# Performance work log

Hardware: AMD Instinct MI355X
Metric: run time of the kernel (lower is better)

The kernel has to match this reference:

```python
import jax, jax.numpy as jnp
import numpy as np


def setup_inputs() -> dict:
    key = jax.random.key(0)
    k1, k2 = jax.random.split(key)
    B, G = 32, 512
    center = jax.random.normal(k1, (B, G, 6), dtype=jnp.float32)
    lrf = jax.random.normal(k2, (B, G, 3, 3), dtype=jnp.float32)
    return {"center": center, "lrf": lrf}


def reference(center, lrf):
    # center: [B, G, 6], lrf: [B, G, 3, 3]
    center_pos = center[:, :, 0:3]                       # [B, G, 3]
    # diff[b, i, j, c] = center_pos[b, j, c] - center_pos[b, i, c]
    diff = center_pos[:, None, :, :] - center_pos[:, :, None, :]  # [B, G, G, 3]
    # rel_pos[b, i, j, k] = sum_c diff[b, i, j, c] * lrf[b, i, c, k]
    rel_pos = jnp.einsum('bijc,bick->bijk', diff, lrf)   # [B, G, G, 3]
    # rel_ori[b, i, j] = lrf[b, i]^T @ lrf[b, j]
    rel_ori = jnp.einsum('bikm,bjkn->bijmn', lrf, lrf)   # [B, G, G, 3, 3]
    return (rel_pos, rel_ori)
```

## Files before the change

kernel.cpp:

```cpp
#include <hip/hip_runtime.h>


#define G_ 512
#define NB 32

__global__ __launch_bounds__(256) void relposori_kernel(
    const float* __restrict__ center,
    const float* __restrict__ lrf,
    float* __restrict__ out_pos,
    float* __restrict__ out_ori)
{
    __shared__ float s[4 * 3072];
    int tid  = threadIdx.x;
    int lane = tid & 63;
    int w    = tid >> 6;
    float* sp = s + w * 3072;
    float* so = sp + 768;

    const int nchunks = NB * G_ * 2;
    const int nwaves  = gridDim.x * 4;
    int cw = blockIdx.x * 4 + w;

    for (int c = cw; c < nchunks; c += nwaves) {
        int bi = c >> 1;
        int b  = bi >> 9;
        int j0 = (c & 1) << 8;

        const float* ci = center + (size_t)bi * 6;
        const float* li = lrf    + (size_t)bi * 9;
        float ci0 = ci[0], ci1 = ci[1], ci2 = ci[2];
        float li_[9];
#pragma unroll
        for (int t = 0; t < 9; ++t) li_[t] = li[t];

#pragma unroll
        for (int q = 0; q < 4; ++q) {
            int jl = (q << 6) + lane;
            size_t bj = (size_t)b * G_ + (size_t)(j0 + jl);
            const float* cj = center + bj * 6;
            const float* lj = lrf    + bj * 9;
            float d0 = cj[0] - ci0, d1 = cj[1] - ci1, d2 = cj[2] - ci2;
            float lj_[9];
#pragma unroll
            for (int t = 0; t < 9; ++t) lj_[t] = lj[t];

#pragma unroll
            for (int k = 0; k < 3; ++k)
                sp[jl * 3 + k] = d0 * li_[k] + d1 * li_[3 + k] + d2 * li_[6 + k];

#pragma unroll
            for (int m = 0; m < 3; ++m)
#pragma unroll
                for (int n = 0; n < 3; ++n)
                    so[jl * 9 + m * 3 + n] = li_[m]     * lj_[n]
                                           + li_[3 + m] * lj_[3 + n]
                                           + li_[6 + m] * lj_[6 + n];
        }

        asm volatile("s_waitcnt lgkmcnt(0)" ::: "memory");
        __builtin_amdgcn_sched_barrier(0);

        size_t row = (size_t)bi * G_ + (size_t)j0;
        const float4* sp4 = (const float4*)sp;
        float4* op4 = (float4*)(out_pos + row * 3);
#pragma unroll
        for (int t = 0; t < 3; ++t)
            op4[(t << 6) + lane] = sp4[(t << 6) + lane];

        const float4* so4 = (const float4*)so;
        float4* oo4 = (float4*)(out_ori + row * 9);
#pragma unroll
        for (int t = 0; t < 9; ++t)
            oo4[(t << 6) + lane] = so4[(t << 6) + lane];

        asm volatile("" ::: "memory");
        __builtin_amdgcn_wave_barrier();
    }
}

extern "C" void kernel_launch(void* const* d_in, const int* in_sizes, int n_in,
                              void* d_out, int out_size, void* d_ws, size_t ws_size,
                              hipStream_t stream) {
    const float* center = (const float*)d_in[0];
    const float* lrf    = (const float*)d_in[1];
    float* out = (float*)d_out;

    const int B = 32;
    const size_t n_pos = (size_t)B * G_ * G_ * 3;
    float* out_pos = out;
    float* out_ori = out + n_pos;

    dim3 grid(512);
    dim3 block(256);
    hipLaunchKernelGGL(relposori_kernel, grid, block, 0, stream,
                       center, lrf, out_pos, out_ori);
}
```

Before: 84.85 us.

## Shrink per-wave chunk to 64 columns to cut LDS and raise occupancy

Each wave now handles 64 j-columns per chunk instead of 256, which cuts per-wave LDS staging from 12KB to 3KB and lets more blocks be resident (launch bounds min 8 blocks). The grid grows to 2048 blocks and the wave id is made scalar with readfirstlane. The output stores become partial-lane float4 writes (48/144 vectors per chunk). In exchange, the row i data is reloaded more often and each chunk carries more loop overhead.

```diff
diff --git a/kernel.cpp b/kernel.cpp
--- a/kernel.cpp
+++ b/kernel.cpp
@@ -4,27 +4,28 @@
 #define G_ 512
 #define NB 32
 
-__global__ __launch_bounds__(256) void relposori_kernel(
+__global__ __launch_bounds__(256, 8) void relposori_kernel(
     const float* __restrict__ center,
     const float* __restrict__ lrf,
     float* __restrict__ out_pos,
     float* __restrict__ out_ori)
 {
-    __shared__ float s[4 * 3072];
+    __shared__ float s[4 * 768];
     int tid  = threadIdx.x;
     int lane = tid & 63;
     int w    = tid >> 6;
-    float* sp = s + w * 3072;
-    float* so = sp + 768;
+    float* sp = s + w * 768;
+    float* so = sp + 192;
 
-    const int nchunks = NB * G_ * 2;
-    const int nwaves  = gridDim.x * 4;
-    int cw = blockIdx.x * 4 + w;
+    const int nchunks = NB * G_ * 8;
+    const int nwaves  = 2048 * 4;
+    int wave_id = __builtin_amdgcn_readfirstlane(blockIdx.x * 4 + w);
 
-    for (int c = cw; c < nchunks; c += nwaves) {
-        int bi = c >> 1;
+    for (int c = wave_id; c < nchunks; c += nwaves) {
+        int bi = c >> 3;
         int b  = bi >> 9;
-        int j0 = (c & 1) << 8;
+        int q  = c & 7;
+        int j0 = q << 6;
 
         const float* ci = center + (size_t)bi * 6;
         const float* li = lrf    + (size_t)bi * 9;
@@ -33,45 +34,39 @@
 #pragma unroll
         for (int t = 0; t < 9; ++t) li_[t] = li[t];
 
+        int j = j0 + lane;
+        size_t bj = (size_t)b * G_ + (size_t)j;
+        const float* cj = center + bj * 6;
+        const float* lj = lrf    + bj * 9;
+        float d0 = cj[0] - ci0, d1 = cj[1] - ci1, d2 = cj[2] - ci2;
+        float lj_[9];
 #pragma unroll
-        for (int q = 0; q < 4; ++q) {
-            int jl = (q << 6) + lane;
-            size_t bj = (size_t)b * G_ + (size_t)(j0 + jl);
-            const float* cj = center + bj * 6;
-            const float* lj = lrf    + bj * 9;
-            float d0 = cj[0] - ci0, d1 = cj[1] - ci1, d2 = cj[2] - ci2;
-            float lj_[9];
-#pragma unroll
-            for (int t = 0; t < 9; ++t) lj_[t] = lj[t];
+        for (int t = 0; t < 9; ++t) lj_[t] = lj[t];
 
 #pragma unroll
-            for (int k = 0; k < 3; ++k)
-                sp[jl * 3 + k] = d0 * li_[k] + d1 * li_[3 + k] + d2 * li_[6 + k];
+        for (int k = 0; k < 3; ++k)
+            sp[lane * 3 + k] = d0 * li_[k] + d1 * li_[3 + k] + d2 * li_[6 + k];
 
 #pragma unroll
-            for (int m = 0; m < 3; ++m)
+        for (int m = 0; m < 3; ++m)
 #pragma unroll
-                for (int n = 0; n < 3; ++n)
-                    so[jl * 9 + m * 3 + n] = li_[m]     * lj_[n]
-                                           + li_[3 + m] * lj_[3 + n]
-                                           + li_[6 + m] * lj_[6 + n];
-        }
+            for (int n = 0; n < 3; ++n)
+                so[lane * 9 + m * 3 + n] = li_[m]     * lj_[n]
+                                         + li_[3 + m] * lj_[3 + n]
+                                         + li_[6 + m] * lj_[6 + n];
 
         asm volatile("s_waitcnt lgkmcnt(0)" ::: "memory");
         __builtin_amdgcn_sched_barrier(0);
 
-        size_t row = (size_t)bi * G_ + (size_t)j0;
         const float4* sp4 = (const float4*)sp;
-        float4* op4 = (float4*)(out_pos + row * 3);
-#pragma unroll
-        for (int t = 0; t < 3; ++t)
-            op4[(t << 6) + lane] = sp4[(t << 6) + lane];
+        const float4* so4 = (const float4*)so;
+        float4* op4 = (float4*)out_pos + ((size_t)bi * 384 + 48 * q);
+        float4* oo4 = (float4*)out_ori + ((size_t)bi * 1152 + 144 * q);
 
-        const float4* so4 = (const float4*)so;
-        float4* oo4 = (float4*)(out_ori + row * 9);
-#pragma unroll
-        for (int t = 0; t < 9; ++t)
-            oo4[(t << 6) + lane] = so4[(t << 6) + lane];
+        if (lane < 48) op4[lane] = sp4[lane];
+        oo4[lane]      = so4[lane];
+        oo4[64 + lane] = so4[64 + lane];
+        if (lane < 16) oo4[128 + lane] = so4[128 + lane];
 
         asm volatile("" ::: "memory");
         __builtin_amdgcn_wave_barrier();
@@ -90,7 +85,7 @@
     float* out_pos = out;
     float* out_ori = out + n_pos;
 
-    dim3 grid(512);
+    dim3 grid(2048);
     dim3 block(256);
     hipLaunchKernelGGL(relposori_kernel, grid, block, 0, stream,
                        center, lrf, out_pos, out_ori);
```

New measurement: 80.68 us. 4.9% less time.
